# Performance work log

Hardware: AMD Instinct MI355X
Metric: run time of the kernel (lower is better)

Reference implementation:

```python
import jax, jax.numpy as jnp
import numpy as np

B, TV, TS, DIN, D = 32, 1024, 64, 1024, 512
EPS = 1e-15


def setup_inputs() -> dict:
    key = jax.random.key(0)
    k1, k2, k3, k4, k5, k6 = jax.random.split(key, 6)
    videos = jax.random.normal(k1, (B, TV, DIN), dtype=jnp.float32)
    sentences = jax.random.normal(k2, (B, TS, DIN), dtype=jnp.float32)
    lengths = jax.random.randint(k3, (B,), 1, TS, dtype=jnp.int32)
    scale = 1.0 / np.sqrt(DIN)
    Wv = jax.random.normal(k4, (DIN, D), dtype=jnp.float32) * scale
    bv = jnp.zeros((D,), dtype=jnp.float32)
    Ws = jax.random.normal(k5, (DIN, D), dtype=jnp.float32) * scale
    bs = jnp.zeros((D,), dtype=jnp.float32)
    return {"videos": videos, "sentences": sentences, "lengths": lengths,
            "Wv": Wv, "bv": bv, "Ws": Ws, "bs": bs}


def _pair_score(V, S):
    # V: [TV, D] video repr for item i; S: [TS, D] sentence repr for item j
    nv = jnp.linalg.norm(V, axis=1)                      # [TV]
    ns = jnp.linalg.norm(S, axis=1)                      # [TS]
    # cosine-similarity coattention matrix via normalized matmul (no repeat/tile)
    C = (V @ S.T) / (nv[:, None] * ns[None, :] + EPS)    # [TV, TS]
    A = jax.nn.softmax(C, axis=1)                        # normalize over sentence axis
    att = A @ S                                          # [TV, D] sentence attention
    num = jnp.sum(V * att, axis=1)                       # [TV]
    den = nv * jnp.linalg.norm(att, axis=1)
    score = num / (den + EPS)                            # [TV] per-frame video score
    return jax.nn.logsumexp(score)                       # scalar


def reference(videos, sentences, lengths, Wv, bv, Ws, bs):
    # per-timestep dense encoders (video_layer / sentence_layer)
    videos_repr = jnp.einsum('btf,fd->btd', videos, Wv) + bv      # [B, TV, D]
    sentences_repr = jnp.einsum('bsf,fd->bsd', sentences, Ws) + bs  # [B, TS, D]
    # all-pairs (i video, j sentence) scores, vectorized over the B x B grid
    pairwise = jax.vmap(lambda V: jax.vmap(lambda S: _pair_score(V, S))(sentences_repr))
    scores_videos = pairwise(videos_repr)                # [B, B]
    return scores_videos
```

## Files before the change

### kernel.cpp

```cpp
#include <hip/hip_runtime.h>
#include <hip/hip_bf16.h>
#include <stdint.h>
#include <math.h>

typedef __attribute__((ext_vector_type(8))) __bf16 bf16x8;
typedef __attribute__((ext_vector_type(4))) float f32x4;

#define B_   32
#define TV_  1024
#define TS_  64
#define DIN_ 1024
#define D_   512

static __device__ __forceinline__ unsigned short f2bf(float f) {
    union { float f; uint32_t u; } x; x.f = f;
    uint32_t r = x.u + 0x7fffu + ((x.u >> 16) & 1u);
    return (unsigned short)(r >> 16);
}
static __device__ __forceinline__ uint32_t cvtpk(float lo, float hi) {
    uint32_t r;
    asm("v_cvt_pk_bf16_f32 %0, %1, %2" : "=v"(r) : "v"(lo), "v"(hi));
    return r;
}
static __device__ __forceinline__ void swap32(uint32_t& a, uint32_t& b) {
    asm volatile("v_permlane32_swap_b32 %0, %1" : "+v"(a), "+v"(b));
}
static __device__ __forceinline__ void swap16(uint32_t& a, uint32_t& b) {
    asm volatile("v_permlane16_swap_b32 %0, %1" : "+v"(a), "+v"(b));
}

__global__ __launch_bounds__(256) void transpose_w(const float* __restrict__ Wv,
                                                   const float* __restrict__ Wsn,
                                                   unsigned short* __restrict__ Wt) {
    const int w = blockIdx.z;
    const float* src = w ? Wsn : Wv;
    __shared__ float t[32][33];
    const int k0 = blockIdx.x * 32, n0 = blockIdx.y * 32;
    const int tx = threadIdx.x & 31, ty = threadIdx.x >> 5;
    #pragma unroll
    for (int r = 0; r < 32; r += 8)
        t[r + ty][tx] = src[(size_t)(k0 + r + ty) * D_ + n0 + tx];
    __syncthreads();
    #pragma unroll
    for (int r = 0; r < 32; r += 8)
        Wt[(size_t)w * 524288 + (size_t)(n0 + r + ty) * DIN_ + k0 + tx] = f2bf(t[tx][r + ty]);
}

__global__ __launch_bounds__(256) void encoder_gemm(const float* __restrict__ X,
                                                    const unsigned short* __restrict__ Wt,
                                                    const float* __restrict__ bias,
                                                    unsigned short* __restrict__ outR,
                                                    int mpx) {
    __shared__ char Asb[128 * 128];
    __shared__ char Bsb[128 * 128];
    const int bid = blockIdx.x;
    const int xcd = bid & 7, sl = bid >> 3;
    const int m0 = (xcd * mpx + (sl >> 2)) * 128;
    const int n0 = (sl & 3) * 128;
    const int tid = threadIdx.x;
    const int lane = tid & 63, wid = tid >> 6;
    const int g = lane >> 4, c = lane & 15;
    const int wm = wid >> 1, wn = wid & 1;

    f32x4 acc[4][4];
    {
        f32x4 z = {0.f, 0.f, 0.f, 0.f};
        #pragma unroll
        for (int a = 0; a < 4; ++a)
            #pragma unroll
            for (int b = 0; b < 4; ++b) acc[a][b] = z;
    }

    for (int kk = 0; kk < 16; ++kk) {
        const int k0 = kk * 64;
        #pragma unroll
        for (int it = 0; it < 8; ++it) {
            int idx = it * 256 + tid;
            int m = idx >> 4, k4 = idx & 15;
            float4 v = *(const float4*)(X + (size_t)(m0 + m) * DIN_ + k0 + k4 * 4);
            uint2 pk;
            pk.x = ((uint32_t)f2bf(v.y) << 16) | f2bf(v.x);
            pk.y = ((uint32_t)f2bf(v.w) << 16) | f2bf(v.z);
            *(uint2*)(Asb + m * 128 + ((k4 * 8) ^ ((m & 7) << 4))) = pk;
        }
        #pragma unroll
        for (int it = 0; it < 4; ++it) {
            int idx = it * 256 + tid;
            int n = idx >> 3, kq = idx & 7;
            uint4 v = *(const uint4*)(Wt + (size_t)(n0 + n) * DIN_ + k0 + kq * 8);
            *(uint4*)(Bsb + n * 128 + ((kq * 16) ^ ((n & 7) << 4))) = v;
        }
        __syncthreads();
        #pragma unroll
        for (int ks = 0; ks < 2; ++ks) {
            bf16x8 a[4], b[4];
            #pragma unroll
            for (int mt = 0; mt < 4; ++mt) {
                int row = wm * 64 + mt * 16 + c;
                a[mt] = *(const bf16x8*)(Asb + row * 128 + ((g * 16 + ks * 64) ^ ((c & 7) << 4)));
            }
            #pragma unroll
            for (int nt = 0; nt < 4; ++nt) {
                int rowb = wn * 64 + nt * 16 + c;
                b[nt] = *(const bf16x8*)(Bsb + rowb * 128 + ((g * 16 + ks * 64) ^ ((c & 7) << 4)));
            }
            #pragma unroll
            for (int mt = 0; mt < 4; ++mt)
                #pragma unroll
                for (int nt = 0; nt < 4; ++nt)
                    acc[mt][nt] = __builtin_amdgcn_mfma_f32_16x16x32_bf16(a[mt], b[nt], acc[mt][nt], 0, 0, 0);
        }
        __syncthreads();
    }
    #pragma unroll
    for (int nt = 0; nt < 4; ++nt) {
        int col = n0 + wn * 64 + nt * 16 + c;
        float bb = bias[col];
        #pragma unroll
        for (int mt = 0; mt < 4; ++mt) {
            int rbase = m0 + wm * 64 + mt * 16 + g * 4;
            #pragma unroll
            for (int r = 0; r < 4; ++r)
                outR[(size_t)(rbase + r) * D_ + col] = f2bf(acc[mt][nt][r] + bb);
        }
    }
}

__global__ __launch_bounds__(256) void rownorm_kernel(const unsigned short* __restrict__ R,
                                                      float* __restrict__ nrm, int nrows) {
    const int row = blockIdx.x * 4 + (threadIdx.x >> 6);
    const int lane = threadIdx.x & 63;
    if (row >= nrows) return;
    uint4 v = ((const uint4*)(R + (size_t)row * D_))[lane];
    float s = 0.f;
    uint32_t wsx[4] = {v.x, v.y, v.z, v.w};
    #pragma unroll
    for (int q = 0; q < 4; ++q) {
        float lo = __uint_as_float(wsx[q] << 16);
        float hi = __uint_as_float(wsx[q] & 0xffff0000u);
        s += lo * lo + hi * hi;
    }
    #pragma unroll
    for (int d = 1; d < 64; d <<= 1) s += __shfl_xor(s, d);
    if (lane == 0) nrm[row] = sqrtf(s);
}

__global__ __launch_bounds__(256) void gram_kernel(const unsigned short* __restrict__ S,
                                                   unsigned short* __restrict__ Gn,
                                                   unsigned short* __restrict__ Sf,
                                                   float* __restrict__ lgns) {
    const int i = blockIdx.x;
    const int tid = threadIdx.x, lane = tid & 63, w = tid >> 6;
    const int g = lane >> 4, c = lane & 15;
    const unsigned short* Sp = S + (size_t)i * TS_ * D_;
    __shared__ float rns_sh[64];

    {
        const int row = tid >> 2, q = tid & 3;
        const uint4* rp = (const uint4*)(Sp + (size_t)row * D_ + q * 128);
        float s = 0.f;
        #pragma unroll
        for (int e = 0; e < 16; ++e) {
            uint4 v = rp[e];
            uint32_t wsx[4] = {v.x, v.y, v.z, v.w};
            #pragma unroll
            for (int qq = 0; qq < 4; ++qq) {
                float lo = __uint_as_float(wsx[qq] << 16);
                float hi = __uint_as_float(wsx[qq] & 0xffff0000u);
                s += lo * lo + hi * hi;
            }
        }
        s += __shfl_xor(s, 1);
        s += __shfl_xor(s, 2);
        if (q == 0) {
            rns_sh[row] = rsqrtf(s);
            lgns[i * 64 + row] = 0.5f * log2f(s);
        }
    }
    __syncthreads();

    {
        f32x4 acc[4];
        {
            f32x4 z = {0.f, 0.f, 0.f, 0.f};
            #pragma unroll
            for (int a = 0; a < 4; ++a) acc[a] = z;
        }
        #pragma unroll
        for (int ks = 0; ks < 16; ++ks) {
            bf16x8 a = *(const bf16x8*)(Sp + (size_t)(w * 16 + c) * D_ + ks * 32 + g * 8);
            #pragma unroll
            for (int nt = 0; nt < 4; ++nt) {
                bf16x8 b = *(const bf16x8*)(Sp + (size_t)(nt * 16 + c) * D_ + ks * 32 + g * 8);
                acc[nt] = __builtin_amdgcn_mfma_f32_16x16x32_bf16(a, b, acc[nt], 0, 0, 0);
            }
        }
        #pragma unroll
        for (int nt = 0; nt < 4; ++nt)
            #pragma unroll
            for (int r = 0; r < 4; ++r) {
                int R = w * 16 + g * 4 + r, C = nt * 16 + c;
                float vn = acc[nt][r] * rns_sh[R] * rns_sh[C];
                int idx = (w * 2 + (nt >> 1)) * 512 + (((nt & 1) * 2 + (c >> 3)) * 16 + g * 4 + r) * 8 + (c & 7);
                Gn[(size_t)i * 4096 + idx] = f2bf(vn);
            }
    }

    #pragma unroll
    for (int t = 0; t < 16; ++t) {
        int idx = t * 256 + tid;
        int ks = idx >> 8, at = (idx >> 6) & 3, ln = idx & 63;
        int row = at * 16 + (ln & 15), gg = ln >> 4;
        uint4 raw = *(const uint4*)(Sp + (size_t)row * D_ + ks * 32 + gg * 8);
        float sc = rns_sh[row];
        uint32_t rw[4] = {raw.x, raw.y, raw.z, raw.w};
        uint4 o;
        uint32_t* op = (uint32_t*)&o;
        #pragma unroll
        for (int q = 0; q < 4; ++q) {
            float lo = __uint_as_float(rw[q] << 16) * sc;
            float hi = __uint_as_float(rw[q] & 0xffff0000u) * sc;
            op[q] = cvtpk(lo, hi);
        }
        *(uint4*)(Sf + (size_t)i * 32768 + idx * 8) = o;
    }
}

__global__ __launch_bounds__(1024, 1) void pairwise_kernel(const unsigned short* __restrict__ V,
                                                           const unsigned short* __restrict__ Sf,
                                                           const unsigned short* __restrict__ Gn,
                                                           const float* __restrict__ nv,
                                                           const float* __restrict__ lgns,
                                                           float* __restrict__ outp) {
    __shared__ char Ssh[131072];
    __shared__ char Gsh[16384];
    __shared__ float lgsh[128];
    __shared__ float wsum[32];

    const int bid = blockIdx.x;
    const int xcd = bid & 7, slot = bid >> 3;
    const int i = xcd + 8 * (slot >> 4);
    const int jp = slot & 15;
    const int tid = threadIdx.x;
    const int lane = tid & 63, w = tid >> 6;
    const int g = lane >> 4, c = lane & 15;
    const float L2E = 1.4426950408889634f;

    {
        const unsigned short* Sjf = Sf + (size_t)jp * 65536;
        #pragma unroll
        for (int it = 0; it < 8; ++it) {
            int idx = it * 1024 + tid;
            *(uint4*)(Ssh + idx * 16) = *(const uint4*)(Sjf + idx * 8);
        }
        *(uint4*)(Gsh + tid * 16) = *(const uint4*)(Gn + (size_t)jp * 8192 + tid * 8);
        if (tid < 32) *(float4*)(lgsh + tid * 4) = *(const float4*)(lgns + jp * 128 + tid * 4);
    }
    __syncthreads();

    const unsigned short* Vb[2];
    #pragma unroll
    for (int mt = 0; mt < 2; ++mt)
        Vb[mt] = V + ((size_t)i * TV_ + w * 32 + mt * 16 + c) * D_ + g * 8;
    const float* nvb = nv + i * TV_ + w * 32 + c;

    float s_run0 = 0.0f, s_run1 = 0.0f;

    for (int chunk = 0; chunk < 2; ++chunk) {
        const size_t coff = (size_t)chunk * 512 * D_;
        f32x4 acc[2][8];
        {
            f32x4 z = {0.f, 0.f, 0.f, 0.f};
            #pragma unroll
            for (int a = 0; a < 2; ++a)
                #pragma unroll
                for (int b = 0; b < 8; ++b) acc[a][b] = z;
        }
        bf16x8 bcur[2], bnxt[2];
        #pragma unroll
        for (int mt = 0; mt < 2; ++mt) bcur[mt] = *(const bf16x8*)(Vb[mt] + coff);
        #pragma unroll
        for (int ks = 0; ks < 16; ++ks) {
            bf16x8 a[8];
            #pragma unroll
            for (int q = 0; q < 8; ++q)
                a[q] = *(const bf16x8*)(Ssh + ((q >> 2) << 16) + (((ks * 4 + (q & 3))) << 10) + lane * 16);
            if (ks < 15) {
                #pragma unroll
                for (int mt = 0; mt < 2; ++mt)
                    bnxt[mt] = *(const bf16x8*)(Vb[mt] + coff + (ks + 1) * 32);
            }
            __builtin_amdgcn_s_setprio(1);
            #pragma unroll
            for (int mt = 0; mt < 2; ++mt)
                #pragma unroll
                for (int q = 0; q < 8; ++q)
                    acc[mt][q] = __builtin_amdgcn_mfma_f32_16x16x32_bf16(a[q], bcur[mt], acc[mt][q], 0, 0, 0);
            __builtin_amdgcn_s_setprio(0);
            #pragma unroll
            for (int mt = 0; mt < 2; ++mt) bcur[mt] = bnxt[mt];
        }

        float nv4[2], rnv[2];
        #pragma unroll
        for (int mt = 0; mt < 2; ++mt) {
            nv4[mt] = nvb[chunk * 512 + mt * 16];
            rnv[mt] = __builtin_amdgcn_rcpf(nv4[mt]);
        }

        #pragma unroll
        for (int jj = 0; jj < 2; ++jj) {
            float lg[16];
            #pragma unroll
            for (int at = 0; at < 4; ++at) {
                float4 t4 = *(const float4*)(lgsh + jj * 64 + at * 16 + g * 4);
                lg[at * 4 + 0] = t4.x; lg[at * 4 + 1] = t4.y;
                lg[at * 4 + 2] = t4.z; lg[at * 4 + 3] = t4.w;
            }
            float SPC[2], SPQ[2] = {0.f, 0.f};
            uint32_t bfr[2][2][4];
            #pragma unroll
            for (int mt = 0; mt < 2; ++mt) {
                float rnvL = rnv[mt] * L2E;
                float SPCm = 0.f;
                #pragma unroll
                for (int at = 0; at < 4; ++at)
                    #pragma unroll
                    for (int r = 0; r < 4; ++r) {
                        float t = acc[mt][jj * 4 + at][r];
                        float e = exp2f(fmaf(t, rnvL, lg[at * 4 + r]));
                        SPCm = fmaf(e, t, SPCm);
                        acc[mt][jj * 4 + at][r] = e;
                    }
                SPC[mt] = SPCm;
                #pragma unroll
                for (int ks2 = 0; ks2 < 2; ++ks2) {
                    const int a0 = jj * 4 + ks2 * 2, a1 = a0 + 1;
                    uint32_t A  = cvtpk(acc[mt][a0][0], acc[mt][a0][1]);
                    uint32_t Bw = cvtpk(acc[mt][a0][2], acc[mt][a0][3]);
                    uint32_t C  = cvtpk(acc[mt][a1][0], acc[mt][a1][1]);
                    uint32_t Dw = cvtpk(acc[mt][a1][2], acc[mt][a1][3]);
                    swap32(A, C);  swap16(A, C);
                    swap32(Bw, Dw); swap16(Bw, Dw);
                    bfr[mt][ks2][0] = A;  bfr[mt][ks2][1] = Bw;
                    bfr[mt][ks2][2] = C;  bfr[mt][ks2][3] = Dw;
                }
            }
            #pragma unroll
            for (int st = 0; st < 4; ++st) {
                bf16x8 g0 = *(const bf16x8*)(Gsh + (jj << 13) + ((st * 2 + 0) << 10) + lane * 16);
                bf16x8 g1 = *(const bf16x8*)(Gsh + (jj << 13) + ((st * 2 + 1) << 10) + lane * 16);
                __builtin_amdgcn_s_setprio(1);
                #pragma unroll
                for (int mt = 0; mt < 2; ++mt) {
                    union { uint32_t u[4]; bf16x8 v; } f0, f1;
                    #pragma unroll
                    for (int q = 0; q < 4; ++q) { f0.u[q] = bfr[mt][0][q]; f1.u[q] = bfr[mt][1][q]; }
                    f32x4 d2 = {0.f, 0.f, 0.f, 0.f};
                    d2 = __builtin_amdgcn_mfma_f32_16x16x32_bf16(g0, f0.v, d2, 0, 0, 0);
                    d2 = __builtin_amdgcn_mfma_f32_16x16x32_bf16(g1, f1.v, d2, 0, 0, 0);
                    #pragma unroll
                    for (int r = 0; r < 4; ++r) SPQ[mt] += acc[mt][jj * 4 + st][r] * d2[r];
                }
                __builtin_amdgcn_s_setprio(0);
            }

            #pragma unroll
            for (int mt = 0; mt < 2; ++mt) {
                float SPCm = SPC[mt], SPQm = SPQ[mt];
                SPCm += __shfl_xor(SPCm, 16); SPCm += __shfl_xor(SPCm, 32);
                SPQm += __shfl_xor(SPQm, 16); SPQm += __shfl_xor(SPQm, 32);
                float sc = SPCm * rnv[mt] * rsqrtf(fmaxf(SPQm, 1e-20f));
                float ev = exp2f(sc * L2E);
                if (jj == 0) s_run0 += ev; else s_run1 += ev;
            }
        }
    }

    #pragma unroll
    for (int d = 1; d < 16; d <<= 1) {
        s_run0 += __shfl_xor(s_run0, d);
        s_run1 += __shfl_xor(s_run1, d);
    }
    if (lane == 0) { wsum[w * 2] = s_run0; wsum[w * 2 + 1] = s_run1; }
    __syncthreads();
    if (tid < 2) {
        float total = 0.f;
        #pragma unroll
        for (int ww = 0; ww < 16; ++ww) total += wsum[ww * 2 + tid];
        outp[i * 32 + jp * 2 + tid] = 0.69314718055994531f * log2f(total);
    }
}

extern "C" void kernel_launch(void* const* d_in, const int* in_sizes, int n_in,
                              void* d_out, int out_size, void* d_ws, size_t ws_size,
                              hipStream_t stream) {
    const float* videos    = (const float*)d_in[0];
    const float* sentences = (const float*)d_in[1];
    const float* Wv  = (const float*)d_in[3];
    const float* bv  = (const float*)d_in[4];
    const float* Wsn = (const float*)d_in[5];
    const float* bs  = (const float*)d_in[6];
    float* outp = (float*)d_out;

    char* ws = (char*)d_ws;
    unsigned short* Vrep = (unsigned short*)(ws);
    unsigned short* Srep = (unsigned short*)(ws + 33554432);
    unsigned short* Wt   = (unsigned short*)(ws + 35651584);
    unsigned short* Gn   = (unsigned short*)(ws + 37748736);
    float*          nv   = (float*)(ws + 38010880);
    float*          lgns = (float*)(ws + 38141952);
    unsigned short* Sf   = Wt;

    transpose_w<<<dim3(32, 16, 2), 256, 0, stream>>>(Wv, Wsn, Wt);
    encoder_gemm<<<1024, 256, 0, stream>>>(videos, Wt, bv, Vrep, 32);
    encoder_gemm<<<64, 256, 0, stream>>>(sentences, Wt + 524288, bs, Srep, 2);
    rownorm_kernel<<<8192, 256, 0, stream>>>(Vrep, nv, B_ * TV_);
    gram_kernel<<<B_, 256, 0, stream>>>(Srep, Gn, Sf, lgns);
    pairwise_kernel<<<512, 1024, 0, stream>>>(Vrep, Sf, Gn, nv, lgns, outp);
}
```

Measured before the change: 208.7 us.

## Halve encoder GEMM N-tile and split pairwise waves across sentence pairs

The encoder GEMM tile is narrowed from 128x128 to 128x64, doubling the grid and adding a 4-blocks-per-SM launch bound. This raises occupancy, at the cost of re-reading (and re-converting) the fp32 activation tile twice as often. The pairwise kernel now assigns each half of its 16 waves to one of the two sentences (jj) instead of having every wave handle both. Each wave now covers 256 video rows per chunk over four chunks, which halves accumulator registers but doubles the V loads issued per block.

```diff
diff --git a/kernel.cpp b/kernel.cpp
--- a/kernel.cpp
+++ b/kernel.cpp
@@ -46,29 +46,29 @@
         Wt[(size_t)w * 524288 + (size_t)(n0 + r + ty) * DIN_ + k0 + tx] = f2bf(t[tx][r + ty]);
 }
 
-__global__ __launch_bounds__(256) void encoder_gemm(const float* __restrict__ X,
-                                                    const unsigned short* __restrict__ Wt,
-                                                    const float* __restrict__ bias,
-                                                    unsigned short* __restrict__ outR,
-                                                    int mpx) {
+__global__ __launch_bounds__(256, 4) void encoder_gemm(const float* __restrict__ X,
+                                                       const unsigned short* __restrict__ Wt,
+                                                       const float* __restrict__ bias,
+                                                       unsigned short* __restrict__ outR,
+                                                       int mpx) {
     __shared__ char Asb[128 * 128];
-    __shared__ char Bsb[128 * 128];
+    __shared__ char Bsb[64 * 128];
     const int bid = blockIdx.x;
     const int xcd = bid & 7, sl = bid >> 3;
-    const int m0 = (xcd * mpx + (sl >> 2)) * 128;
-    const int n0 = (sl & 3) * 128;
+    const int m0 = (xcd * mpx + (sl >> 3)) * 128;
+    const int n0 = (sl & 7) * 64;
     const int tid = threadIdx.x;
     const int lane = tid & 63, wid = tid >> 6;
     const int g = lane >> 4, c = lane & 15;
     const int wm = wid >> 1, wn = wid & 1;
 
-    f32x4 acc[4][4];
+    f32x4 acc[4][2];
     {
         f32x4 z = {0.f, 0.f, 0.f, 0.f};
         #pragma unroll
         for (int a = 0; a < 4; ++a)
             #pragma unroll
-            for (int b = 0; b < 4; ++b) acc[a][b] = z;
+            for (int b = 0; b < 2; ++b) acc[a][b] = z;
     }
 
     for (int kk = 0; kk < 16; ++kk) {
@@ -84,7 +84,7 @@
             *(uint2*)(Asb + m * 128 + ((k4 * 8) ^ ((m & 7) << 4))) = pk;
         }
         #pragma unroll
-        for (int it = 0; it < 4; ++it) {
+        for (int it = 0; it < 2; ++it) {
             int idx = it * 256 + tid;
             int n = idx >> 3, kq = idx & 7;
             uint4 v = *(const uint4*)(Wt + (size_t)(n0 + n) * DIN_ + k0 + kq * 8);
@@ -93,28 +93,28 @@
         __syncthreads();
         #pragma unroll
         for (int ks = 0; ks < 2; ++ks) {
-            bf16x8 a[4], b[4];
+            bf16x8 a[4], b[2];
             #pragma unroll
             for (int mt = 0; mt < 4; ++mt) {
                 int row = wm * 64 + mt * 16 + c;
                 a[mt] = *(const bf16x8*)(Asb + row * 128 + ((g * 16 + ks * 64) ^ ((c & 7) << 4)));
             }
             #pragma unroll
-            for (int nt = 0; nt < 4; ++nt) {
-                int rowb = wn * 64 + nt * 16 + c;
+            for (int nt = 0; nt < 2; ++nt) {
+                int rowb = wn * 32 + nt * 16 + c;
                 b[nt] = *(const bf16x8*)(Bsb + rowb * 128 + ((g * 16 + ks * 64) ^ ((c & 7) << 4)));
             }
             #pragma unroll
             for (int mt = 0; mt < 4; ++mt)
                 #pragma unroll
-                for (int nt = 0; nt < 4; ++nt)
+                for (int nt = 0; nt < 2; ++nt)
                     acc[mt][nt] = __builtin_amdgcn_mfma_f32_16x16x32_bf16(a[mt], b[nt], acc[mt][nt], 0, 0, 0);
         }
         __syncthreads();
     }
     #pragma unroll
-    for (int nt = 0; nt < 4; ++nt) {
-        int col = n0 + wn * 64 + nt * 16 + c;
+    for (int nt = 0; nt < 2; ++nt) {
+        int col = n0 + wn * 32 + nt * 16 + c;
         float bb = bias[col];
         #pragma unroll
         for (int mt = 0; mt < 4; ++mt) {
@@ -235,7 +235,7 @@
     __shared__ char Ssh[131072];
     __shared__ char Gsh[16384];
     __shared__ float lgsh[128];
-    __shared__ float wsum[32];
+    __shared__ float wsum[16];
 
     const int bid = blockIdx.x;
     const int xcd = bid & 7, slot = bid >> 3;
@@ -243,6 +243,7 @@
     const int jp = slot & 15;
     const int tid = threadIdx.x;
     const int lane = tid & 63, w = tid >> 6;
+    const int jj = w >> 3, wv = w & 7;
     const int g = lane >> 4, c = lane & 15;
     const float L2E = 1.4426950408889634f;
 
@@ -256,35 +257,43 @@
         *(uint4*)(Gsh + tid * 16) = *(const uint4*)(Gn + (size_t)jp * 8192 + tid * 8);
         if (tid < 32) *(float4*)(lgsh + tid * 4) = *(const float4*)(lgns + jp * 128 + tid * 4);
     }
+
     __syncthreads();
+    float lg[16];
+    #pragma unroll
+    for (int at = 0; at < 4; ++at) {
+        float4 t4 = *(const float4*)(lgsh + jj * 64 + at * 16 + g * 4);
+        lg[at * 4 + 0] = t4.x; lg[at * 4 + 1] = t4.y;
+        lg[at * 4 + 2] = t4.z; lg[at * 4 + 3] = t4.w;
+    }
 
     const unsigned short* Vb[2];
     #pragma unroll
     for (int mt = 0; mt < 2; ++mt)
-        Vb[mt] = V + ((size_t)i * TV_ + w * 32 + mt * 16 + c) * D_ + g * 8;
-    const float* nvb = nv + i * TV_ + w * 32 + c;
-
-    float s_run0 = 0.0f, s_run1 = 0.0f;
-
-    for (int chunk = 0; chunk < 2; ++chunk) {
-        const size_t coff = (size_t)chunk * 512 * D_;
-        f32x4 acc[2][8];
+        Vb[mt] = V + ((size_t)i * TV_ + wv * 32 + mt * 16 + c) * D_ + g * 8;
+    const float* nvb = nv + i * TV_ + wv * 32 + c;
+
+    float s_run = 0.0f;
+
+    for (int chunk = 0; chunk < 4; ++chunk) {
+        const size_t coff = (size_t)chunk * 256 * D_;
+        f32x4 acc[2][4];
         {
             f32x4 z = {0.f, 0.f, 0.f, 0.f};
             #pragma unroll
             for (int a = 0; a < 2; ++a)
                 #pragma unroll
-                for (int b = 0; b < 8; ++b) acc[a][b] = z;
+                for (int b = 0; b < 4; ++b) acc[a][b] = z;
         }
         bf16x8 bcur[2], bnxt[2];
         #pragma unroll
         for (int mt = 0; mt < 2; ++mt) bcur[mt] = *(const bf16x8*)(Vb[mt] + coff);
         #pragma unroll
         for (int ks = 0; ks < 16; ++ks) {
-            bf16x8 a[8];
-            #pragma unroll
-            for (int q = 0; q < 8; ++q)
-                a[q] = *(const bf16x8*)(Ssh + ((q >> 2) << 16) + (((ks * 4 + (q & 3))) << 10) + lane * 16);
+            bf16x8 a[4];
+            #pragma unroll
+            for (int q = 0; q < 4; ++q)
+                a[q] = *(const bf16x8*)(Ssh + (jj << 16) + ((ks * 4 + q) << 10) + lane * 16);
             if (ks < 15) {
                 #pragma unroll
                 for (int mt = 0; mt < 2; ++mt)
@@ -294,100 +303,81 @@
             #pragma unroll
             for (int mt = 0; mt < 2; ++mt)
                 #pragma unroll
-                for (int q = 0; q < 8; ++q)
+                for (int q = 0; q < 4; ++q)
                     acc[mt][q] = __builtin_amdgcn_mfma_f32_16x16x32_bf16(a[q], bcur[mt], acc[mt][q], 0, 0, 0);
             __builtin_amdgcn_s_setprio(0);
             #pragma unroll
             for (int mt = 0; mt < 2; ++mt) bcur[mt] = bnxt[mt];
         }
 
-        float nv4[2], rnv[2];
+        float SPC[2], SPQ[2] = {0.f, 0.f}, rnv[2], nv4[2];
+        uint32_t bfr[2][2][4];
         #pragma unroll
         for (int mt = 0; mt < 2; ++mt) {
-            nv4[mt] = nvb[chunk * 512 + mt * 16];
+            nv4[mt] = nvb[chunk * 256 + mt * 16];
             rnv[mt] = __builtin_amdgcn_rcpf(nv4[mt]);
-        }
-
-        #pragma unroll
-        for (int jj = 0; jj < 2; ++jj) {
-            float lg[16];
-            #pragma unroll
-            for (int at = 0; at < 4; ++at) {
-                float4 t4 = *(const float4*)(lgsh + jj * 64 + at * 16 + g * 4);
-                lg[at * 4 + 0] = t4.x; lg[at * 4 + 1] = t4.y;
-                lg[at * 4 + 2] = t4.z; lg[at * 4 + 3] = t4.w;
-            }
-            float SPC[2], SPQ[2] = {0.f, 0.f};
-            uint32_t bfr[2][2][4];
+            float rnvL = rnv[mt] * L2E;
+            float SPCm = 0.f;
+            #pragma unroll
+            for (int at = 0; at < 4; ++at)
+                #pragma unroll
+                for (int r = 0; r < 4; ++r) {
+                    float t = acc[mt][at][r];
+                    float e = exp2f(fmaf(t, rnvL, lg[at * 4 + r]));
+                    SPCm = fmaf(e, t, SPCm);
+                    acc[mt][at][r] = e;
+                }
+            SPC[mt] = SPCm;
+            #pragma unroll
+            for (int ks2 = 0; ks2 < 2; ++ks2) {
+                const int a0 = ks2 * 2, a1 = a0 + 1;
+                uint32_t A  = cvtpk(acc[mt][a0][0], acc[mt][a0][1]);
+                uint32_t Bw = cvtpk(acc[mt][a0][2], acc[mt][a0][3]);
+                uint32_t C  = cvtpk(acc[mt][a1][0], acc[mt][a1][1]);
+                uint32_t Dw = cvtpk(acc[mt][a1][2], acc[mt][a1][3]);
+                swap32(A, C);  swap16(A, C);
+                swap32(Bw, Dw); swap16(Bw, Dw);
+                bfr[mt][ks2][0] = A;  bfr[mt][ks2][1] = Bw;
+                bfr[mt][ks2][2] = C;  bfr[mt][ks2][3] = Dw;
+            }
+        }
+        #pragma unroll
+        for (int st = 0; st < 4; ++st) {
+            bf16x8 g0 = *(const bf16x8*)(Gsh + (jj << 13) + ((st * 2 + 0) << 10) + lane * 16);
+            bf16x8 g1 = *(const bf16x8*)(Gsh + (jj << 13) + ((st * 2 + 1) << 10) + lane * 16);
+            __builtin_amdgcn_s_setprio(1);
             #pragma unroll
             for (int mt = 0; mt < 2; ++mt) {
-                float rnvL = rnv[mt] * L2E;
-                float SPCm = 0.f;
-                #pragma unroll
-                for (int at = 0; at < 4; ++at)
-                    #pragma unroll
-                    for (int r = 0; r < 4; ++r) {
-                        float t = acc[mt][jj * 4 + at][r];
-                        float e = exp2f(fmaf(t, rnvL, lg[at * 4 + r]));
-                        SPCm = fmaf(e, t, SPCm);
-                        acc[mt][jj * 4 + at][r] = e;
-                    }
-                SPC[mt] = SPCm;
-                #pragma unroll
-                for (int ks2 = 0; ks2 < 2; ++ks2) {
-                    const int a0 = jj * 4 + ks2 * 2, a1 = a0 + 1;
-                    uint32_t A  = cvtpk(acc[mt][a0][0], acc[mt][a0][1]);
-                    uint32_t Bw = cvtpk(acc[mt][a0][2], acc[mt][a0][3]);
-                    uint32_t C  = cvtpk(acc[mt][a1][0], acc[mt][a1][1]);
-                    uint32_t Dw = cvtpk(acc[mt][a1][2], acc[mt][a1][3]);
-                    swap32(A, C);  swap16(A, C);
-                    swap32(Bw, Dw); swap16(Bw, Dw);
-                    bfr[mt][ks2][0] = A;  bfr[mt][ks2][1] = Bw;
-                    bfr[mt][ks2][2] = C;  bfr[mt][ks2][3] = Dw;
-                }
-            }
-            #pragma unroll
-            for (int st = 0; st < 4; ++st) {
-                bf16x8 g0 = *(const bf16x8*)(Gsh + (jj << 13) + ((st * 2 + 0) << 10) + lane * 16);
-                bf16x8 g1 = *(const bf16x8*)(Gsh + (jj << 13) + ((st * 2 + 1) << 10) + lane * 16);
-                __builtin_amdgcn_s_setprio(1);
-                #pragma unroll
-                for (int mt = 0; mt < 2; ++mt) {
-                    union { uint32_t u[4]; bf16x8 v; } f0, f1;
-                    #pragma unroll
-                    for (int q = 0; q < 4; ++q) { f0.u[q] = bfr[mt][0][q]; f1.u[q] = bfr[mt][1][q]; }
-                    f32x4 d2 = {0.f, 0.f, 0.f, 0.f};
-                    d2 = __builtin_amdgcn_mfma_f32_16x16x32_bf16(g0, f0.v, d2, 0, 0, 0);
-                    d2 = __builtin_amdgcn_mfma_f32_16x16x32_bf16(g1, f1.v, d2, 0, 0, 0);
-                    #pragma unroll
-                    for (int r = 0; r < 4; ++r) SPQ[mt] += acc[mt][jj * 4 + st][r] * d2[r];
-                }
-                __builtin_amdgcn_s_setprio(0);
-            }
-
-            #pragma unroll
-            for (int mt = 0; mt < 2; ++mt) {
-                float SPCm = SPC[mt], SPQm = SPQ[mt];
-                SPCm += __shfl_xor(SPCm, 16); SPCm += __shfl_xor(SPCm, 32);
-                SPQm += __shfl_xor(SPQm, 16); SPQm += __shfl_xor(SPQm, 32);
-                float sc = SPCm * rnv[mt] * rsqrtf(fmaxf(SPQm, 1e-20f));
-                float ev = exp2f(sc * L2E);
-                if (jj == 0) s_run0 += ev; else s_run1 += ev;
-            }
-        }
-    }
-
-    #pragma unroll
-    for (int d = 1; d < 16; d <<= 1) {
-        s_run0 += __shfl_xor(s_run0, d);
-        s_run1 += __shfl_xor(s_run1, d);
-    }
-    if (lane == 0) { wsum[w * 2] = s_run0; wsum[w * 2 + 1] = s_run1; }
+                union { uint32_t u[4]; bf16x8 v; } f0, f1;
+                #pragma unroll
+                for (int q = 0; q < 4; ++q) { f0.u[q] = bfr[mt][0][q]; f1.u[q] = bfr[mt][1][q]; }
+                f32x4 d2 = {0.f, 0.f, 0.f, 0.f};
+                d2 = __builtin_amdgcn_mfma_f32_16x16x32_bf16(g0, f0.v, d2, 0, 0, 0);
+                d2 = __builtin_amdgcn_mfma_f32_16x16x32_bf16(g1, f1.v, d2, 0, 0, 0);
+                #pragma unroll
+                for (int r = 0; r < 4; ++r) SPQ[mt] += acc[mt][st][r] * d2[r];
+            }
+            __builtin_amdgcn_s_setprio(0);
+        }
+
+        #pragma unroll
+        for (int mt = 0; mt < 2; ++mt) {
+            float SPCm = SPC[mt], SPQm = SPQ[mt];
+            SPCm += __shfl_xor(SPCm, 16); SPCm += __shfl_xor(SPCm, 32);
+            SPQm += __shfl_xor(SPQm, 16); SPQm += __shfl_xor(SPQm, 32);
+            float sc = SPCm * rnv[mt] * rsqrtf(fmaxf(SPQm, 1e-20f));
+            s_run += exp2f(sc * L2E);
+        }
+    }
+
+    #pragma unroll
+    for (int d = 1; d < 16; d <<= 1) s_run += __shfl_xor(s_run, d);
+    if (lane == 0) wsum[w] = s_run;
     __syncthreads();
     if (tid < 2) {
         float total = 0.f;
         #pragma unroll
-        for (int ww = 0; ww < 16; ++ww) total += wsum[ww * 2 + tid];
+        for (int k = 0; k < 8; ++k) total += wsum[tid * 8 + k];
         outp[i * 32 + jp * 2 + tid] = 0.69314718055994531f * log2f(total);
     }
 }
@@ -413,8 +403,8 @@
     unsigned short* Sf   = Wt;
 
     transpose_w<<<dim3(32, 16, 2), 256, 0, stream>>>(Wv, Wsn, Wt);
-    encoder_gemm<<<1024, 256, 0, stream>>>(videos, Wt, bv, Vrep, 32);
-    encoder_gemm<<<64, 256, 0, stream>>>(sentences, Wt + 524288, bs, Srep, 2);
+    encoder_gemm<<<2048, 256, 0, stream>>>(videos, Wt, bv, Vrep, 32);
+    encoder_gemm<<<128, 256, 0, stream>>>(sentences, Wt + 524288, bs, Srep, 2);
     rownorm_kernel<<<8192, 256, 0, stream>>>(Vrep, nv, B_ * TV_);
     gram_kernel<<<B_, 256, 0, stream>>>(Srep, Gn, Sf, lgns);
     pairwise_kernel<<<512, 1024, 0, stream>>>(Vrep, Sf, Gn, nv, lgns, outp);
```

Result: slower. 297.9 us (+42.8%).
